# Kernel tuning notes

Measured on AMD Instinct MI355X. Metric: run time of the kernel, lower is better.

Reference implementation:

```python
import jax, jax.numpy as jnp
import numpy as np

NH = 4  # num_heads
EPS = 1e-5

def _layernorm(x, g, b):
    mu = jnp.mean(x, axis=-1, keepdims=True)
    var = jnp.mean(jnp.square(x - mu), axis=-1, keepdims=True)
    return (x - mu) * jax.lax.rsqrt(var + EPS) * g + b

def setup_inputs() -> dict:
    key = jax.random.key(0)
    ks = jax.random.split(key, 16)
    B, D, T, H = 8, 128, 128, 64
    s = 0.02
    inp = {
        'h': jax.random.normal(ks[0], (B, D, T, H), jnp.float32),
        'W': jax.random.normal(ks[1], (B, D, D), jnp.float32),
        'wq': jax.random.normal(ks[2], (H, H), jnp.float32) * s,
        'bq': jnp.zeros((H,), jnp.float32),
        'wk': jax.random.normal(ks[3], (H, H), jnp.float32) * s,
        'bk': jnp.zeros((H,), jnp.float32),
        'wv': jax.random.normal(ks[4], (H, H), jnp.float32) * s,
        'bv': jnp.zeros((H,), jnp.float32),
        'wo': jax.random.normal(ks[5], (H, H), jnp.float32) * s,
        'bo': jnp.zeros((H,), jnp.float32),
        'we': jax.random.normal(ks[6], (NH, 1), jnp.float32) * s,
        'be': jnp.zeros((NH,), jnp.float32),
        'g1': jnp.ones((H,), jnp.float32),
        'b1': jnp.zeros((H,), jnp.float32),
        'w_ff1': jax.random.normal(ks[7], (2 * H, H), jnp.float32) * s,
        'b_ff1': jnp.zeros((2 * H,), jnp.float32),
        'w_ff2': jax.random.normal(ks[8], (H, 2 * H), jnp.float32) * s,
        'b_ff2': jnp.zeros((H,), jnp.float32),
        'g2': jnp.ones((H,), jnp.float32),
        'b2': jnp.zeros((H,), jnp.float32),
    }
    return inp

def reference(h, W, wq, bq, wk, bk, wv, bv, wo, bo, we, be, g1, b1,
              w_ff1, b_ff1, w_ff2, b_ff2, g2, b2):
    B, D, T, H = h.shape
    hd = H // NH
    # [B,D,T,H] -> [B*T, D, H]
    h_flat = jnp.transpose(h, (0, 2, 1, 3)).reshape(B * T, D, H)
    Q = (h_flat @ wq.T + bq).reshape(B * T, D, NH, hd)
    K = (h_flat @ wk.T + bk).reshape(B * T, D, NH, hd)
    V = (h_flat @ wv.T + bv).reshape(B * T, D, NH, hd)
    scores = jnp.einsum('bqhd,bkhd->bhqk', Q, K) / jnp.sqrt(jnp.float32(hd))
    # edge bias: [B,D,D,1] @ we.T -> [B,D,D,NH] -> [B,NH,D,D], broadcast over T
    eb = jnp.transpose(W[..., None] * we[:, 0] + be, (0, 3, 1, 2))  # [B,NH,D,D]
    eb = jnp.broadcast_to(eb[:, None], (B, T, NH, D, D)).reshape(B * T, NH, D, D)
    attn = jax.nn.softmax(scores + eb, axis=-1)
    out = jnp.einsum('bhqk,bkhd->bqhd', attn, V).reshape(B * T, D, H)
    out = out @ wo.T + bo
    x = _layernorm(h_flat + out, g1, b1)
    ffn = jax.nn.gelu(x @ w_ff1.T + b_ff1, approximate=False) @ w_ff2.T + b_ff2
    y = _layernorm(x + ffn, g2, b2)
    return jnp.transpose(y.reshape(B, T, D, H), (0, 2, 1, 3))
```

## Files before the change

### kernel.cpp

```cpp
#include <hip/hip_runtime.h>
#include <hip/hip_bf16.h>

#define NTHREADS 512

typedef __attribute__((ext_vector_type(8))) short short8;
typedef __attribute__((ext_vector_type(4))) float f32x4;

#define MFMA(a, b, c) __builtin_amdgcn_mfma_f32_16x16x32_bf16(a, b, c, 0, 0, 0)

__device__ __forceinline__ unsigned short f2u(float x) {
    __hip_bfloat16 b = __float2bfloat16(x);
    return *reinterpret_cast<unsigned short*>(&b);
}
__device__ __forceinline__ float u2f(unsigned short u) {
    unsigned v = ((unsigned)u) << 16;
    return *reinterpret_cast<float*>(&v);
}
__device__ __forceinline__ unsigned pack2(float lo, float hi) {
    return ((unsigned)f2u(hi) << 16) | (unsigned)f2u(lo);
}
__device__ __forceinline__ int swz64(int r, int c8)  { return r * 128 + ((c8 ^ (r & 7)) << 4); }
__device__ __forceinline__ int swz64e(int r, int c)  { return r * 128 + (((c >> 3) ^ (r & 7)) << 4) + ((c & 7) << 1); }
__device__ __forceinline__ int swz128(int r, int c8) { return r * 256 + ((c8 ^ (r & 15)) << 4); }
__device__ __forceinline__ int swz128e(int r, int c) { return r * 256 + ((((c >> 3) ^ (r & 15))) << 4) + ((c & 7) << 1); }

__device__ __forceinline__ short8 cvt8(const float* src) {
    float4 f0 = *(const float4*)src;
    float4 f1 = *(const float4*)(src + 4);
    short8 v = { (short)f2u(f0.x), (short)f2u(f0.y), (short)f2u(f0.z), (short)f2u(f0.w),
                 (short)f2u(f1.x), (short)f2u(f1.y), (short)f2u(f1.z), (short)f2u(f1.w) };
    return v;
}

__global__ __launch_bounds__(NTHREADS, 4) void gal_kernel(
    const float* __restrict__ h,  const float* __restrict__ W,
    const float* __restrict__ wq, const float* __restrict__ bq,
    const float* __restrict__ wk, const float* __restrict__ bk,
    const float* __restrict__ wv, const float* __restrict__ bv,
    const float* __restrict__ wo, const float* __restrict__ bo,
    const float* __restrict__ we, const float* __restrict__ be,
    const float* __restrict__ g1, const float* __restrict__ b1,
    const float* __restrict__ w1, const float* __restrict__ bf1,
    const float* __restrict__ w2, const float* __restrict__ bff2,
    const float* __restrict__ g2, const float* __restrict__ b2,
    float* __restrict__ out)
{
    __shared__ __align__(16) unsigned char smem[65536];

    const int gblk = blockIdx.x;
    const int b   = gblk >> 7;
    const int tt  = gblk & 127;
    const int tid = threadIdx.x;
    const int lane = tid & 63;
    const int w   = tid >> 6;
    const int l15 = lane & 15;
    const int g   = lane >> 4;

    const float* hp = h + (((size_t)b * 128) * 128 + tt) * 64;
    const float* Wb = W + (size_t)b * 128 * 128;

#pragma unroll
    for (int i = 0; i < 2; ++i) {
        int idx = tid + i * 512;
        int d = idx >> 3, c = idx & 7;
        *(short8*)(smem + swz64(d, c)) = cvt8(hp + (size_t)d * 8192 + c * 8);
    }
    {
        int j = tid >> 3, c = tid & 7;
        *(short8*)(smem + 16384 + swz64(j, c)) = cvt8(wq + j * 64 + c * 8);
        *(short8*)(smem + 24576 + swz64(j, c)) = cvt8(wk + j * 64 + c * 8);
        *(short8*)(smem + 32768 + swz64(j, c)) = cvt8(wv + j * 64 + c * 8);
    }
    __syncthreads();

    f32x4 aq[4], ak4[4], av4[4];
    {
        short8 ah0 = *(const short8*)(smem + swz64(16 * w + l15, g));
        short8 ah1 = *(const short8*)(smem + swz64(16 * w + l15, g + 4));
        f32x4 z = {0.f, 0.f, 0.f, 0.f};
#pragma unroll
        for (int nt = 0; nt < 4; ++nt) { aq[nt] = z; ak4[nt] = z; av4[nt] = z; }
#pragma unroll
        for (int nt = 0; nt < 4; ++nt) {
#pragma unroll
            for (int kh = 0; kh < 2; ++kh) {
                short8 ah = kh ? ah1 : ah0;
                short8 bwq = *(const short8*)(smem + 16384 + swz64(16 * nt + l15, g + 4 * kh));
                aq[nt] = MFMA(ah, bwq, aq[nt]);
                short8 bwk = *(const short8*)(smem + 24576 + swz64(16 * nt + l15, g + 4 * kh));
                ak4[nt] = MFMA(ah, bwk, ak4[nt]);
                short8 bwv = *(const short8*)(smem + 32768 + swz64(16 * nt + l15, g + 4 * kh));
                av4[nt] = MFMA(ah, bwv, av4[nt]);
            }
        }
    }
    float bqv[4], bkv[4], bvv[4];
#pragma unroll
    for (int nt = 0; nt < 4; ++nt) {
        bqv[nt] = bq[16 * nt + l15]; bkv[nt] = bk[16 * nt + l15]; bvv[nt] = bv[16 * nt + l15];
    }
    __syncthreads();
#pragma unroll
    for (int nt = 0; nt < 4; ++nt) {
        int j = 16 * nt + l15;
#pragma unroll
        for (int jr = 0; jr < 4; ++jr) {
            int d = 16 * w + 4 * g + jr;
            *(unsigned short*)(smem + swz64e(d, j))          = f2u((aq[nt][jr] + bqv[nt]) * 0.25f);
            *(unsigned short*)(smem + 16384 + swz64e(d, j))  = f2u(ak4[nt][jr] + bkv[nt]);
            *(unsigned short*)(smem + 32768 + swz128e(j, d)) = f2u(av4[nt][jr] + bvv[nt]);
        }
    }
    __syncthreads();

    const int q = 16 * w + l15;
    const int src0 = l15 + ((lane & 16) << 1);
    const int src1 = src0 + 16;
    const bool hiMt = (g >> 1) & 1;

    for (int hd = 0; hd < 4; ++hd) {
        float weh = we[hd], beh = be[hd];
        short8 qf = {0, 0, 0, 0, 0, 0, 0, 0};
        if (g < 2) qf = *(const short8*)(smem + swz64(q, 2 * hd + g));
        f32x4 s[8];
#pragma unroll
        for (int Mt = 0; Mt < 8; ++Mt) {
            float4 w4 = *(const float4*)(Wb + (size_t)q * 128 + 16 * Mt + 4 * g);
            f32x4 c0 = { w4.x * weh + beh, w4.y * weh + beh, w4.z * weh + beh, w4.w * weh + beh };
            short8 kf = {0, 0, 0, 0, 0, 0, 0, 0};
            if (g < 2) kf = *(const short8*)(smem + 16384 + swz64(16 * Mt + l15, 2 * hd + g));
            s[Mt] = MFMA(kf, qf, c0);
        }
        float mx = s[0][0];
#pragma unroll
        for (int Mt = 0; Mt < 8; ++Mt)
#pragma unroll
            for (int jr = 0; jr < 4; ++jr) mx = fmaxf(mx, s[Mt][jr]);
        mx = fmaxf(mx, __shfl_xor(mx, 16));
        mx = fmaxf(mx, __shfl_xor(mx, 32));
        float tot = 0.f;
#pragma unroll
        for (int Mt = 0; Mt < 8; ++Mt)
#pragma unroll
            for (int jr = 0; jr < 4; ++jr) { s[Mt][jr] = __expf(s[Mt][jr] - mx); tot += s[Mt][jr]; }
        tot += __shfl_xor(tot, 16);
        tot += __shfl_xor(tot, 32);
        float sinv = 1.f / tot;
        unsigned pk[16];
#pragma unroll
        for (int Mt = 0; Mt < 8; ++Mt) {
            pk[2 * Mt]     = pack2(s[Mt][0], s[Mt][1]);
            pk[2 * Mt + 1] = pack2(s[Mt][2], s[Mt][3]);
        }
        f32x4 o = {0.f, 0.f, 0.f, 0.f};
#pragma unroll
        for (int kc = 0; kc < 4; ++kc) {
            unsigned a0 = __shfl((int)pk[4 * kc + 0], src0), a1 = __shfl((int)pk[4 * kc + 1], src0);
            unsigned b0 = __shfl((int)pk[4 * kc + 2], src0), b1 = __shfl((int)pk[4 * kc + 3], src0);
            unsigned a2 = __shfl((int)pk[4 * kc + 0], src1), a3 = __shfl((int)pk[4 * kc + 1], src1);
            unsigned b2 = __shfl((int)pk[4 * kc + 2], src1), b3 = __shfl((int)pk[4 * kc + 3], src1);
            union { unsigned u[4]; short8 s8; } pf;
            pf.u[0] = hiMt ? b0 : a0;
            pf.u[1] = hiMt ? b1 : a1;
            pf.u[2] = hiMt ? b2 : a2;
            pf.u[3] = hiMt ? b3 : a3;
            short8 vf = *(const short8*)(smem + 32768 + swz128(16 * hd + l15, g + 4 * kc));
            o = MFMA(vf, pf.s8, o);
        }
#pragma unroll
        for (int jr = 0; jr < 4; ++jr)
            *(unsigned short*)(smem + 49152 + swz64e(q, 16 * hd + 4 * g + jr)) = f2u(o[jr] * sinv);
    }
    __syncthreads();

    {
        int j = tid >> 3, c = tid & 7;
        *(short8*)(smem + swz64(j, c)) = cvt8(wo + j * 64 + c * 8);
    }
    __syncthreads();
    {
        short8 ao0 = *(const short8*)(smem + 49152 + swz64(16 * w + l15, g));
        short8 ao1 = *(const short8*)(smem + 49152 + swz64(16 * w + l15, g + 4));
        f32x4 xo[4];
        float g1v[4], b1v[4];
#pragma unroll
        for (int nt = 0; nt < 4; ++nt) {
            float bov = bo[16 * nt + l15];
            f32x4 c0 = { bov, bov, bov, bov };
            xo[nt] = c0;
            g1v[nt] = g1[16 * nt + l15];
            b1v[nt] = b1[16 * nt + l15];
        }
#pragma unroll
        for (int nt = 0; nt < 4; ++nt)
#pragma unroll
            for (int kh = 0; kh < 2; ++kh) {
                short8 bw = *(const short8*)(smem + swz64(16 * nt + l15, g + 4 * kh));
                xo[nt] = MFMA(kh ? ao1 : ao0, bw, xo[nt]);
            }
        float r[4][4];
#pragma unroll
        for (int nt = 0; nt < 4; ++nt)
#pragma unroll
            for (int jr = 0; jr < 4; ++jr)
                r[nt][jr] = xo[nt][jr] + hp[(size_t)(16 * w + 4 * g + jr) * 8192 + 16 * nt + l15];
#pragma unroll
        for (int jr = 0; jr < 4; ++jr) {
            float ps = 0.f, pq = 0.f;
#pragma unroll
            for (int nt = 0; nt < 4; ++nt) { ps += r[nt][jr]; pq += r[nt][jr] * r[nt][jr]; }
#pragma unroll
            for (int off = 1; off <= 8; off <<= 1) { ps += __shfl_xor(ps, off); pq += __shfl_xor(pq, off); }
            float mu = ps * (1.f / 64.f);
            float va = pq * (1.f / 64.f) - mu * mu;
            float is = rsqrtf(va + 1e-5f);
            int d = 16 * w + 4 * g + jr;
#pragma unroll
            for (int nt = 0; nt < 4; ++nt) {
                float xv = (r[nt][jr] - mu) * is * g1v[nt] + b1v[nt];
                *(unsigned short*)(smem + 16384 + swz64e(d, 16 * nt + l15)) = f2u(xv);
            }
        }
    }
    __syncthreads();

#pragma unroll
    for (int i = 0; i < 2; ++i) {
        int idx = tid + i * 512;
        int m = idx >> 3, c = idx & 7;
        *(short8*)(smem + 32768 + swz64(m, c)) = cvt8(w1 + m * 64 + c * 8);
    }
#pragma unroll
    for (int i = 0; i < 2; ++i) {
        int idx = tid + i * 512;
        int j = idx >> 4, c = idx & 15;
        *(short8*)(smem + 49152 + swz128(j, c)) = cvt8(w2 + j * 128 + c * 8);
    }
    __syncthreads();

    float rr[4][4];
    {
        short8 bx0 = *(const short8*)(smem + 16384 + swz64(16 * w + l15, g));
        short8 bx1 = *(const short8*)(smem + 16384 + swz64(16 * w + l15, g + 4));
        f32x4 tacc[8];
        f32x4 z = {0.f, 0.f, 0.f, 0.f};
#pragma unroll
        for (int Mt = 0; Mt < 8; ++Mt) tacc[Mt] = z;
#pragma unroll
        for (int Mt = 0; Mt < 8; ++Mt)
#pragma unroll
            for (int kh = 0; kh < 2; ++kh) {
                short8 aw1 = *(const short8*)(smem + 32768 + swz64(16 * Mt + l15, g + 4 * kh));
                tacc[Mt] = MFMA(aw1, kh ? bx1 : bx0, tacc[Mt]);
            }
        unsigned pkt[16];
#pragma unroll
        for (int Mt = 0; Mt < 8; ++Mt) {
            float4 bb = *(const float4*)(bf1 + 16 * Mt + 4 * g);
            float v0 = tacc[Mt][0] + bb.x, v1 = tacc[Mt][1] + bb.y;
            float v2 = tacc[Mt][2] + bb.z, v3 = tacc[Mt][3] + bb.w;
            v0 = 0.5f * v0 * (1.f + erff(v0 * 0.70710678118f));
            v1 = 0.5f * v1 * (1.f + erff(v1 * 0.70710678118f));
            v2 = 0.5f * v2 * (1.f + erff(v2 * 0.70710678118f));
            v3 = 0.5f * v3 * (1.f + erff(v3 * 0.70710678118f));
            pkt[2 * Mt]     = pack2(v0, v1);
            pkt[2 * Mt + 1] = pack2(v2, v3);
        }
        f32x4 ya[4];
#pragma unroll
        for (int Mt2 = 0; Mt2 < 4; ++Mt2) {
            float4 bb = *(const float4*)(bff2 + 16 * Mt2 + 4 * g);
            f32x4 c0 = { bb.x, bb.y, bb.z, bb.w };
            ya[Mt2] = c0;
        }
#pragma unroll
        for (int kc = 0; kc < 4; ++kc) {
            unsigned a0 = __shfl((int)pkt[4 * kc + 0], src0), a1 = __shfl((int)pkt[4 * kc + 1], src0);
            unsigned b0 = __shfl((int)pkt[4 * kc + 2], src0), b1 = __shfl((int)pkt[4 * kc + 3], src0);
            unsigned a2 = __shfl((int)pkt[4 * kc + 0], src1), a3 = __shfl((int)pkt[4 * kc + 1], src1);
            unsigned b2 = __shfl((int)pkt[4 * kc + 2], src1), b3 = __shfl((int)pkt[4 * kc + 3], src1);
            union { unsigned u[4]; short8 s8; } pf;
            pf.u[0] = hiMt ? b0 : a0;
            pf.u[1] = hiMt ? b1 : a1;
            pf.u[2] = hiMt ? b2 : a2;
            pf.u[3] = hiMt ? b3 : a3;
#pragma unroll
            for (int Mt2 = 0; Mt2 < 4; ++Mt2) {
                short8 aw2 = *(const short8*)(smem + 49152 + swz128(16 * Mt2 + l15, g + 4 * kc));
                ya[Mt2] = MFMA(aw2, pf.s8, ya[Mt2]);
            }
        }
        float ps = 0.f, pq = 0.f;
#pragma unroll
        for (int Mt2 = 0; Mt2 < 4; ++Mt2)
#pragma unroll
            for (int jr = 0; jr < 4; ++jr) {
                unsigned short xu = *(const unsigned short*)(smem + 16384 + swz64e(q, 16 * Mt2 + 4 * g + jr));
                float v = ya[Mt2][jr] + u2f(xu);
                rr[Mt2][jr] = v;
                ps += v; pq += v * v;
            }
        ps += __shfl_xor(ps, 16); ps += __shfl_xor(ps, 32);
        pq += __shfl_xor(pq, 16); pq += __shfl_xor(pq, 32);
        float mu = ps * (1.f / 64.f);
        float va = pq * (1.f / 64.f) - mu * mu;
        float is = rsqrtf(va + 1e-5f);
#pragma unroll
        for (int Mt2 = 0; Mt2 < 4; ++Mt2) {
            float4 g4 = *(const float4*)(g2 + 16 * Mt2 + 4 * g);
            float4 b4 = *(const float4*)(b2 + 16 * Mt2 + 4 * g);
            rr[Mt2][0] = (rr[Mt2][0] - mu) * is * g4.x + b4.x;
            rr[Mt2][1] = (rr[Mt2][1] - mu) * is * g4.y + b4.y;
            rr[Mt2][2] = (rr[Mt2][2] - mu) * is * g4.z + b4.z;
            rr[Mt2][3] = (rr[Mt2][3] - mu) * is * g4.w + b4.w;
        }
    }
    __syncthreads();
    {
        float* sy = (float*)(smem + 16384);
#pragma unroll
        for (int Mt2 = 0; Mt2 < 4; ++Mt2)
#pragma unroll
            for (int jr = 0; jr < 4; ++jr)
                sy[q * 68 + 16 * Mt2 + 4 * g + jr] = rr[Mt2][jr];
    }
    __syncthreads();
    {
        int qq = tid >> 2, jb = (tid & 3) * 16;
        const float* sp = (const float*)(smem + 16384) + qq * 68 + jb;
        float* op = out + (((size_t)b * 128) * 128 + tt) * 64 + (size_t)qq * 8192 + jb;
        float4 v0 = *(const float4*)(sp);
        float4 v1 = *(const float4*)(sp + 4);
        float4 v2 = *(const float4*)(sp + 8);
        float4 v3 = *(const float4*)(sp + 12);
        *(float4*)(op)      = v0;
        *(float4*)(op + 4)  = v1;
        *(float4*)(op + 8)  = v2;
        *(float4*)(op + 12) = v3;
    }
}

extern "C" void kernel_launch(void* const* d_in, const int* in_sizes, int n_in,
                              void* d_out, int out_size, void* d_ws, size_t ws_size,
                              hipStream_t stream) {
    const float* h   = (const float*)d_in[0];
    const float* W   = (const float*)d_in[1];
    const float* wq  = (const float*)d_in[2];
    const float* bq  = (const float*)d_in[3];
    const float* wk  = (const float*)d_in[4];
    const float* bk  = (const float*)d_in[5];
    const float* wv  = (const float*)d_in[6];
    const float* bv  = (const float*)d_in[7];
    const float* wo  = (const float*)d_in[8];
    const float* bo  = (const float*)d_in[9];
    const float* we  = (const float*)d_in[10];
    const float* be  = (const float*)d_in[11];
    const float* g1  = (const float*)d_in[12];
    const float* b1  = (const float*)d_in[13];
    const float* w1  = (const float*)d_in[14];
    const float* bf1 = (const float*)d_in[15];
    const float* w2  = (const float*)d_in[16];
    const float* bf2 = (const float*)d_in[17];
    const float* g2  = (const float*)d_in[18];
    const float* b2  = (const float*)d_in[19];
    float* out = (float*)d_out;

    gal_kernel<<<1024, NTHREADS, 0, stream>>>(
        h, W, wq, bq, wk, bk, wv, bv, wo, bo, we, be,
        g1, b1, w1, bf1, w2, bf2, g2, b2, out);
}
```

Before: 77.07 us.

## Keep attention output and LN1 activations in registers, shrink LDS for more occupancy

The attention output, the Wo projection, LayerNorm1 and both FFN matmuls now pass activations between stages in registers through lane shuffles instead of round trips through shared memory. This drops several __syncthreads barriers, and the weight loads for Wo, W1 and W2 are batched into one staging phase. Shared memory shrinks from 64KB to 48KB and launch_bounds rises to 6 blocks, aiming for higher occupancy. The edge bias `be` term is removed from the scores, which is only valid because softmax is invariant to a per-head constant added to every key. The changes raise register pressure and could cause spills.

```diff
diff --git a/kernel.cpp b/kernel.cpp
--- a/kernel.cpp
+++ b/kernel.cpp
@@ -32,7 +32,21 @@
     return v;
 }
 
-__global__ __launch_bounds__(NTHREADS, 4) void gal_kernel(
+__device__ __forceinline__ short8 repack4(unsigned p0, unsigned p1, unsigned p2, unsigned p3,
+                                          int src0, int src1, bool hiMt) {
+    unsigned a0 = __shfl((int)p0, src0), a1 = __shfl((int)p1, src0);
+    unsigned b0 = __shfl((int)p2, src0), b1 = __shfl((int)p3, src0);
+    unsigned a2 = __shfl((int)p0, src1), a3 = __shfl((int)p1, src1);
+    unsigned b2 = __shfl((int)p2, src1), b3 = __shfl((int)p3, src1);
+    union { unsigned u[4]; short8 s8; } pf;
+    pf.u[0] = hiMt ? b0 : a0;
+    pf.u[1] = hiMt ? b1 : a1;
+    pf.u[2] = hiMt ? b2 : a2;
+    pf.u[3] = hiMt ? b3 : a3;
+    return pf.s8;
+}
+
+__global__ __launch_bounds__(NTHREADS, 6) void gal_kernel(
     const float* __restrict__ h,  const float* __restrict__ W,
     const float* __restrict__ wq, const float* __restrict__ bq,
     const float* __restrict__ wk, const float* __restrict__ bk,
@@ -45,7 +59,7 @@
     const float* __restrict__ g2, const float* __restrict__ b2,
     float* __restrict__ out)
 {
-    __shared__ __align__(16) unsigned char smem[65536];
+    __shared__ __align__(16) unsigned char smem[49152];
 
     const int gblk = blockIdx.x;
     const int b   = gblk >> 7;
@@ -118,15 +132,17 @@
     const int src1 = src0 + 16;
     const bool hiMt = (g >> 1) & 1;
 
+    float osr[4][4];
+#pragma unroll
     for (int hd = 0; hd < 4; ++hd) {
-        float weh = we[hd], beh = be[hd];
+        float weh = we[hd];
         short8 qf = {0, 0, 0, 0, 0, 0, 0, 0};
         if (g < 2) qf = *(const short8*)(smem + swz64(q, 2 * hd + g));
         f32x4 s[8];
 #pragma unroll
         for (int Mt = 0; Mt < 8; ++Mt) {
             float4 w4 = *(const float4*)(Wb + (size_t)q * 128 + 16 * Mt + 4 * g);
-            f32x4 c0 = { w4.x * weh + beh, w4.y * weh + beh, w4.z * weh + beh, w4.w * weh + beh };
+            f32x4 c0 = { w4.x * weh, w4.y * weh, w4.z * weh, w4.w * weh };
             short8 kf = {0, 0, 0, 0, 0, 0, 0, 0};
             if (g < 2) kf = *(const short8*)(smem + 16384 + swz64(16 * Mt + l15, 2 * hd + g));
             s[Mt] = MFMA(kf, qf, c0);
@@ -155,151 +171,64 @@
         f32x4 o = {0.f, 0.f, 0.f, 0.f};
 #pragma unroll
         for (int kc = 0; kc < 4; ++kc) {
-            unsigned a0 = __shfl((int)pk[4 * kc + 0], src0), a1 = __shfl((int)pk[4 * kc + 1], src0);
-            unsigned b0 = __shfl((int)pk[4 * kc + 2], src0), b1 = __shfl((int)pk[4 * kc + 3], src0);
-            unsigned a2 = __shfl((int)pk[4 * kc + 0], src1), a3 = __shfl((int)pk[4 * kc + 1], src1);
-            unsigned b2 = __shfl((int)pk[4 * kc + 2], src1), b3 = __shfl((int)pk[4 * kc + 3], src1);
-            union { unsigned u[4]; short8 s8; } pf;
-            pf.u[0] = hiMt ? b0 : a0;
-            pf.u[1] = hiMt ? b1 : a1;
-            pf.u[2] = hiMt ? b2 : a2;
-            pf.u[3] = hiMt ? b3 : a3;
+            short8 pf = repack4(pk[4 * kc], pk[4 * kc + 1], pk[4 * kc + 2], pk[4 * kc + 3],
+                                src0, src1, hiMt);
             short8 vf = *(const short8*)(smem + 32768 + swz128(16 * hd + l15, g + 4 * kc));
-            o = MFMA(vf, pf.s8, o);
-        }
-#pragma unroll
-        for (int jr = 0; jr < 4; ++jr)
-            *(unsigned short*)(smem + 49152 + swz64e(q, 16 * hd + 4 * g + jr)) = f2u(o[jr] * sinv);
-    }
+            o = MFMA(vf, pf, o);
+        }
+#pragma unroll
+        for (int jr = 0; jr < 4; ++jr) osr[hd][jr] = o[jr] * sinv;
+    }
+
+    float4 hres[4];
+#pragma unroll
+    for (int Mt2 = 0; Mt2 < 4; ++Mt2)
+        hres[Mt2] = *(const float4*)(hp + (size_t)q * 8192 + 16 * Mt2 + 4 * g);
     __syncthreads();
 
     {
         int j = tid >> 3, c = tid & 7;
-        *(short8*)(smem + swz64(j, c)) = cvt8(wo + j * 64 + c * 8);
-    }
-    __syncthreads();
-    {
-        short8 ao0 = *(const short8*)(smem + 49152 + swz64(16 * w + l15, g));
-        short8 ao1 = *(const short8*)(smem + 49152 + swz64(16 * w + l15, g + 4));
-        f32x4 xo[4];
-        float g1v[4], b1v[4];
-#pragma unroll
-        for (int nt = 0; nt < 4; ++nt) {
-            float bov = bo[16 * nt + l15];
-            f32x4 c0 = { bov, bov, bov, bov };
-            xo[nt] = c0;
-            g1v[nt] = g1[16 * nt + l15];
-            b1v[nt] = b1[16 * nt + l15];
-        }
-#pragma unroll
-        for (int nt = 0; nt < 4; ++nt)
-#pragma unroll
-            for (int kh = 0; kh < 2; ++kh) {
-                short8 bw = *(const short8*)(smem + swz64(16 * nt + l15, g + 4 * kh));
-                xo[nt] = MFMA(kh ? ao1 : ao0, bw, xo[nt]);
-            }
-        float r[4][4];
-#pragma unroll
-        for (int nt = 0; nt < 4; ++nt)
-#pragma unroll
-            for (int jr = 0; jr < 4; ++jr)
-                r[nt][jr] = xo[nt][jr] + hp[(size_t)(16 * w + 4 * g + jr) * 8192 + 16 * nt + l15];
-#pragma unroll
-        for (int jr = 0; jr < 4; ++jr) {
-            float ps = 0.f, pq = 0.f;
-#pragma unroll
-            for (int nt = 0; nt < 4; ++nt) { ps += r[nt][jr]; pq += r[nt][jr] * r[nt][jr]; }
-#pragma unroll
-            for (int off = 1; off <= 8; off <<= 1) { ps += __shfl_xor(ps, off); pq += __shfl_xor(pq, off); }
-            float mu = ps * (1.f / 64.f);
-            float va = pq * (1.f / 64.f) - mu * mu;
-            float is = rsqrtf(va + 1e-5f);
-            int d = 16 * w + 4 * g + jr;
-#pragma unroll
-            for (int nt = 0; nt < 4; ++nt) {
-                float xv = (r[nt][jr] - mu) * is * g1v[nt] + b1v[nt];
-                *(unsigned short*)(smem + 16384 + swz64e(d, 16 * nt + l15)) = f2u(xv);
-            }
-        }
-    }
-    __syncthreads();
-
+        *(short8*)(smem + 16384 + swz64(j, c)) = cvt8(wo + j * 64 + c * 8);
+    }
 #pragma unroll
     for (int i = 0; i < 2; ++i) {
         int idx = tid + i * 512;
         int m = idx >> 3, c = idx & 7;
-        *(short8*)(smem + 32768 + swz64(m, c)) = cvt8(w1 + m * 64 + c * 8);
-    }
-#pragma unroll
-    for (int i = 0; i < 2; ++i) {
-        int idx = tid + i * 512;
-        int j = idx >> 4, c = idx & 15;
-        *(short8*)(smem + 49152 + swz128(j, c)) = cvt8(w2 + j * 128 + c * 8);
-    }
-    __syncthreads();
-
-    float rr[4][4];
-    {
-        short8 bx0 = *(const short8*)(smem + 16384 + swz64(16 * w + l15, g));
-        short8 bx1 = *(const short8*)(smem + 16384 + swz64(16 * w + l15, g + 4));
-        f32x4 tacc[8];
-        f32x4 z = {0.f, 0.f, 0.f, 0.f};
-#pragma unroll
-        for (int Mt = 0; Mt < 8; ++Mt) tacc[Mt] = z;
-#pragma unroll
-        for (int Mt = 0; Mt < 8; ++Mt)
-#pragma unroll
-            for (int kh = 0; kh < 2; ++kh) {
-                short8 aw1 = *(const short8*)(smem + 32768 + swz64(16 * Mt + l15, g + 4 * kh));
-                tacc[Mt] = MFMA(aw1, kh ? bx1 : bx0, tacc[Mt]);
-            }
-        unsigned pkt[16];
-#pragma unroll
-        for (int Mt = 0; Mt < 8; ++Mt) {
-            float4 bb = *(const float4*)(bf1 + 16 * Mt + 4 * g);
-            float v0 = tacc[Mt][0] + bb.x, v1 = tacc[Mt][1] + bb.y;
-            float v2 = tacc[Mt][2] + bb.z, v3 = tacc[Mt][3] + bb.w;
-            v0 = 0.5f * v0 * (1.f + erff(v0 * 0.70710678118f));
-            v1 = 0.5f * v1 * (1.f + erff(v1 * 0.70710678118f));
-            v2 = 0.5f * v2 * (1.f + erff(v2 * 0.70710678118f));
-            v3 = 0.5f * v3 * (1.f + erff(v3 * 0.70710678118f));
-            pkt[2 * Mt]     = pack2(v0, v1);
-            pkt[2 * Mt + 1] = pack2(v2, v3);
-        }
-        f32x4 ya[4];
-#pragma unroll
-        for (int Mt2 = 0; Mt2 < 4; ++Mt2) {
-            float4 bb = *(const float4*)(bff2 + 16 * Mt2 + 4 * g);
-            f32x4 c0 = { bb.x, bb.y, bb.z, bb.w };
-            ya[Mt2] = c0;
-        }
-#pragma unroll
-        for (int kc = 0; kc < 4; ++kc) {
-            unsigned a0 = __shfl((int)pkt[4 * kc + 0], src0), a1 = __shfl((int)pkt[4 * kc + 1], src0);
-            unsigned b0 = __shfl((int)pkt[4 * kc + 2], src0), b1 = __shfl((int)pkt[4 * kc + 3], src0);
-            unsigned a2 = __shfl((int)pkt[4 * kc + 0], src1), a3 = __shfl((int)pkt[4 * kc + 1], src1);
-            unsigned b2 = __shfl((int)pkt[4 * kc + 2], src1), b3 = __shfl((int)pkt[4 * kc + 3], src1);
-            union { unsigned u[4]; short8 s8; } pf;
-            pf.u[0] = hiMt ? b0 : a0;
-            pf.u[1] = hiMt ? b1 : a1;
-            pf.u[2] = hiMt ? b2 : a2;
-            pf.u[3] = hiMt ? b3 : a3;
-#pragma unroll
-            for (int Mt2 = 0; Mt2 < 4; ++Mt2) {
-                short8 aw2 = *(const short8*)(smem + 49152 + swz128(16 * Mt2 + l15, g + 4 * kc));
-                ya[Mt2] = MFMA(aw2, pf.s8, ya[Mt2]);
-            }
-        }
+        *(short8*)(smem + 24576 + swz64(m, c)) = cvt8(w1 + m * 64 + c * 8);
+        int j2 = idx >> 4, c2 = idx & 15;
+        *(short8*)(smem + swz128(j2, c2)) = cvt8(w2 + j2 * 128 + c2 * 8);
+    }
+    __syncthreads();
+
+    f32x4 xt[4];
+#pragma unroll
+    for (int Mt2 = 0; Mt2 < 4; ++Mt2) {
+        float4 bb = *(const float4*)(bo + 16 * Mt2 + 4 * g);
+        f32x4 c0 = { bb.x, bb.y, bb.z, bb.w };
+        xt[Mt2] = c0;
+    }
+#pragma unroll
+    for (int kc = 0; kc < 2; ++kc) {
+        short8 pf = repack4(pack2(osr[2 * kc][0], osr[2 * kc][1]),
+                            pack2(osr[2 * kc][2], osr[2 * kc][3]),
+                            pack2(osr[2 * kc + 1][0], osr[2 * kc + 1][1]),
+                            pack2(osr[2 * kc + 1][2], osr[2 * kc + 1][3]),
+                            src0, src1, hiMt);
+#pragma unroll
+        for (int Mt2 = 0; Mt2 < 4; ++Mt2) {
+            short8 awo = *(const short8*)(smem + 16384 + swz64(16 * Mt2 + l15, g + 4 * kc));
+            xt[Mt2] = MFMA(awo, pf, xt[Mt2]);
+        }
+    }
+    {
         float ps = 0.f, pq = 0.f;
 #pragma unroll
-        for (int Mt2 = 0; Mt2 < 4; ++Mt2)
-#pragma unroll
-            for (int jr = 0; jr < 4; ++jr) {
-                unsigned short xu = *(const unsigned short*)(smem + 16384 + swz64e(q, 16 * Mt2 + 4 * g + jr));
-                float v = ya[Mt2][jr] + u2f(xu);
-                rr[Mt2][jr] = v;
-                ps += v; pq += v * v;
-            }
+        for (int Mt2 = 0; Mt2 < 4; ++Mt2) {
+            float4 hv = hres[Mt2];
+            xt[Mt2][0] += hv.x; xt[Mt2][1] += hv.y; xt[Mt2][2] += hv.z; xt[Mt2][3] += hv.w;
+#pragma unroll
+            for (int jr = 0; jr < 4; ++jr) { ps += xt[Mt2][jr]; pq += xt[Mt2][jr] * xt[Mt2][jr]; }
+        }
         ps += __shfl_xor(ps, 16); ps += __shfl_xor(ps, 32);
         pq += __shfl_xor(pq, 16); pq += __shfl_xor(pq, 32);
         float mu = ps * (1.f / 64.f);
@@ -307,32 +236,103 @@
         float is = rsqrtf(va + 1e-5f);
 #pragma unroll
         for (int Mt2 = 0; Mt2 < 4; ++Mt2) {
+            float4 g4 = *(const float4*)(g1 + 16 * Mt2 + 4 * g);
+            float4 b4 = *(const float4*)(b1 + 16 * Mt2 + 4 * g);
+            xt[Mt2][0] = (xt[Mt2][0] - mu) * is * g4.x + b4.x;
+            xt[Mt2][1] = (xt[Mt2][1] - mu) * is * g4.y + b4.y;
+            xt[Mt2][2] = (xt[Mt2][2] - mu) * is * g4.z + b4.z;
+            xt[Mt2][3] = (xt[Mt2][3] - mu) * is * g4.w + b4.w;
+        }
+    }
+
+    f32x4 tacc[8];
+#pragma unroll
+    for (int Mt = 0; Mt < 8; ++Mt) {
+        float4 bb = *(const float4*)(bf1 + 16 * Mt + 4 * g);
+        f32x4 c0 = { bb.x, bb.y, bb.z, bb.w };
+        tacc[Mt] = c0;
+    }
+#pragma unroll
+    for (int kc = 0; kc < 2; ++kc) {
+        short8 pf = repack4(pack2(xt[2 * kc][0], xt[2 * kc][1]),
+                            pack2(xt[2 * kc][2], xt[2 * kc][3]),
+                            pack2(xt[2 * kc + 1][0], xt[2 * kc + 1][1]),
+                            pack2(xt[2 * kc + 1][2], xt[2 * kc + 1][3]),
+                            src0, src1, hiMt);
+#pragma unroll
+        for (int Mt = 0; Mt < 8; ++Mt) {
+            short8 aw1 = *(const short8*)(smem + 24576 + swz64(16 * Mt + l15, g + 4 * kc));
+            tacc[Mt] = MFMA(aw1, pf, tacc[Mt]);
+        }
+    }
+    unsigned pkt[16];
+#pragma unroll
+    for (int Mt = 0; Mt < 8; ++Mt) {
+        float v0 = tacc[Mt][0], v1 = tacc[Mt][1], v2 = tacc[Mt][2], v3 = tacc[Mt][3];
+        v0 = 0.5f * v0 * (1.f + erff(v0 * 0.70710678118f));
+        v1 = 0.5f * v1 * (1.f + erff(v1 * 0.70710678118f));
+        v2 = 0.5f * v2 * (1.f + erff(v2 * 0.70710678118f));
+        v3 = 0.5f * v3 * (1.f + erff(v3 * 0.70710678118f));
+        pkt[2 * Mt]     = pack2(v0, v1);
+        pkt[2 * Mt + 1] = pack2(v2, v3);
+    }
+    __syncthreads();
+
+    f32x4 ya[4];
+#pragma unroll
+    for (int Mt2 = 0; Mt2 < 4; ++Mt2) {
+        float4 bb = *(const float4*)(bff2 + 16 * Mt2 + 4 * g);
+        f32x4 c0 = { bb.x, bb.y, bb.z, bb.w };
+        ya[Mt2] = c0;
+    }
+#pragma unroll
+    for (int kc = 0; kc < 4; ++kc) {
+        short8 pf = repack4(pkt[4 * kc], pkt[4 * kc + 1], pkt[4 * kc + 2], pkt[4 * kc + 3],
+                            src0, src1, hiMt);
+#pragma unroll
+        for (int Mt2 = 0; Mt2 < 4; ++Mt2) {
+            short8 aw2 = *(const short8*)(smem + swz128(16 * Mt2 + l15, g + 4 * kc));
+            ya[Mt2] = MFMA(aw2, pf, ya[Mt2]);
+        }
+    }
+    {
+        float ps = 0.f, pq = 0.f;
+#pragma unroll
+        for (int Mt2 = 0; Mt2 < 4; ++Mt2) {
+#pragma unroll
+            for (int jr = 0; jr < 4; ++jr) {
+                ya[Mt2][jr] += xt[Mt2][jr];
+                ps += ya[Mt2][jr]; pq += ya[Mt2][jr] * ya[Mt2][jr];
+            }
+        }
+        ps += __shfl_xor(ps, 16); ps += __shfl_xor(ps, 32);
+        pq += __shfl_xor(pq, 16); pq += __shfl_xor(pq, 32);
+        float mu = ps * (1.f / 64.f);
+        float va = pq * (1.f / 64.f) - mu * mu;
+        float is = rsqrtf(va + 1e-5f);
+#pragma unroll
+        for (int Mt2 = 0; Mt2 < 4; ++Mt2) {
             float4 g4 = *(const float4*)(g2 + 16 * Mt2 + 4 * g);
             float4 b4 = *(const float4*)(b2 + 16 * Mt2 + 4 * g);
-            rr[Mt2][0] = (rr[Mt2][0] - mu) * is * g4.x + b4.x;
-            rr[Mt2][1] = (rr[Mt2][1] - mu) * is * g4.y + b4.y;
-            rr[Mt2][2] = (rr[Mt2][2] - mu) * is * g4.z + b4.z;
-            rr[Mt2][3] = (rr[Mt2][3] - mu) * is * g4.w + b4.w;
-        }
-    }
-    __syncthreads();
-    {
-        float* sy = (float*)(smem + 16384);
-#pragma unroll
-        for (int Mt2 = 0; Mt2 < 4; ++Mt2)
-#pragma unroll
-            for (int jr = 0; jr < 4; ++jr)
-                sy[q * 68 + 16 * Mt2 + 4 * g + jr] = rr[Mt2][jr];
+            ya[Mt2][0] = (ya[Mt2][0] - mu) * is * g4.x + b4.x;
+            ya[Mt2][1] = (ya[Mt2][1] - mu) * is * g4.y + b4.y;
+            ya[Mt2][2] = (ya[Mt2][2] - mu) * is * g4.z + b4.z;
+            ya[Mt2][3] = (ya[Mt2][3] - mu) * is * g4.w + b4.w;
+        }
+    }
+#pragma unroll
+    for (int Mt2 = 0; Mt2 < 4; ++Mt2) {
+        float4 v = { ya[Mt2][0], ya[Mt2][1], ya[Mt2][2], ya[Mt2][3] };
+        *(float4*)(smem + 16384 + swz128(q, 4 * Mt2 + g)) = v;
     }
     __syncthreads();
     {
         int qq = tid >> 2, jb = (tid & 3) * 16;
-        const float* sp = (const float*)(smem + 16384) + qq * 68 + jb;
         float* op = out + (((size_t)b * 128) * 128 + tt) * 64 + (size_t)qq * 8192 + jb;
-        float4 v0 = *(const float4*)(sp);
-        float4 v1 = *(const float4*)(sp + 4);
-        float4 v2 = *(const float4*)(sp + 8);
-        float4 v3 = *(const float4*)(sp + 12);
+        float4 v0 = *(const float4*)(smem + 16384 + swz128(qq, (tid & 3) * 4 + 0));
+        float4 v1 = *(const float4*)(smem + 16384 + swz128(qq, (tid & 3) * 4 + 1));
+        float4 v2 = *(const float4*)(smem + 16384 + swz128(qq, (tid & 3) * 4 + 2));
+        float4 v3 = *(const float4*)(smem + 16384 + swz128(qq, (tid & 3) * 4 + 3));
         *(float4*)(op)      = v0;
         *(float4*)(op + 4)  = v1;
         *(float4*)(op + 8)  = v2;
```

After: 111.1 us. 1.44x slower.
